# Kernel tuning notes

Measured on AMD Instinct MI355X. Metric: run time of the kernel, lower is better.

## Reference

```python
import jax, jax.numpy as jnp
import numpy as np

N = 10000      # nodes
E = 160000     # edges (before self-loops)
H = 8          # heads
D_IN, D_H1, D_H2 = 165, 128, 1    # per-head channels of gat1 / gat2
HID = H * D_H1                    # 1024


def batchnorm(x, gamma, beta, eps=1e-5):
    # training-mode BatchNorm1d: biased batch statistics over the node axis
    mu = x.mean(0)
    var = x.var(0)
    return (x - mu) * jax.lax.rsqrt(var + eps) * gamma + beta


def gatv2(x, src, dst, Wl, bl, Wr, br, att, bias, heads, out_ch, concat, n_nodes):
    # PyG GATv2Conv: lin_l on source, lin_r on target; e = att . LeakyReLU(xl_j + xr_i)
    xl = (x @ Wl + bl).reshape(n_nodes, heads, out_ch)   # source transform
    xr = (x @ Wr + br).reshape(n_nodes, heads, out_ch)   # target transform
    e = jax.nn.leaky_relu(xl[src] + xr[dst], 0.2)        # [E,H,C]
    logits = jnp.einsum('ehc,hc->eh', e, att)            # [E,H]
    # segment softmax over incoming edges of each destination node
    m = jax.lax.stop_gradient(jax.ops.segment_max(logits, dst, num_segments=n_nodes))
    a = jnp.exp(logits - m[dst])
    s = jax.ops.segment_sum(a, dst, num_segments=n_nodes)
    alpha = a / (s[dst] + 1e-16)                          # [E,H]
    out = jax.ops.segment_sum(xl[src] * alpha[..., None], dst, num_segments=n_nodes)
    out = out.reshape(n_nodes, heads * out_ch) if concat else out.mean(1)
    return out + bias


def setup_inputs() -> dict:
    key = jax.random.key(0)
    ks = jax.random.split(key, 12)
    g = lambda k, shape, fan_in: jax.random.normal(k, shape, jnp.float32) * (1.0 / np.sqrt(fan_in))
    return {
        'x': jax.random.normal(ks[0], (N, D_IN), jnp.float32),
        'gamma1': jnp.ones((D_IN,), jnp.float32),
        'beta1': jnp.zeros((D_IN,), jnp.float32),
        'Wl1': g(ks[1], (D_IN, HID), D_IN),
        'bl1': jnp.zeros((HID,), jnp.float32),
        'Wr1': g(ks[2], (D_IN, HID), D_IN),
        'br1': jnp.zeros((HID,), jnp.float32),
        'att1': g(ks[3], (H, D_H1), D_H1),
        'bias1': jnp.zeros((HID,), jnp.float32),
        'gamma2': jnp.ones((HID,), jnp.float32),
        'beta2': jnp.zeros((HID,), jnp.float32),
        'Wl2': g(ks[4], (HID, H * D_H2), HID),
        'bl2': jnp.zeros((H * D_H2,), jnp.float32),
        'Wr2': g(ks[5], (HID, H * D_H2), HID),
        'br2': jnp.zeros((H * D_H2,), jnp.float32),
        'att2': g(ks[6], (H, D_H2), D_H2),
        'bias2': jnp.zeros((D_H2,), jnp.float32),
        'edge_index': jax.random.randint(ks[7], (2, E), 0, N, jnp.int64 if jax.config.jax_enable_x64 else jnp.int32),
    }


def reference(x, gamma1, beta1, Wl1, bl1, Wr1, br1, att1, bias1,
              gamma2, beta2, Wl2, bl2, Wr2, br2, att2, bias2, edge_index):
    loops = jnp.arange(N, dtype=edge_index.dtype)
    src = jnp.concatenate([edge_index[0], loops])   # add_self_loops=True (PyG default)
    dst = jnp.concatenate([edge_index[1], loops])
    h = batchnorm(x, gamma1, beta1)
    h = gatv2(h, src, dst, Wl1, bl1, Wr1, br1, att1, bias1, H, D_H1, True, N)
    h = batchnorm(h, gamma2, beta2)
    h = jax.nn.leaky_relu(h, 0.01)                  # F.leaky_relu default slope
    out = gatv2(h, src, dst, Wl2, bl2, Wr2, br2, att2, bias2, H, D_H2, False, N)
    return out
```

## Files before the change

### kernel.cpp

```cpp
#include <hip/hip_runtime.h>

#define NN   10000
#define E0   160000
#define ET   170000
#define DIN  165
#define KP   192
#define HID  1024
#define NH   8
#define BP   200
#define K2P  1032
#define YT   2


typedef __bf16 bf16x8 __attribute__((ext_vector_type(8)));
typedef float  f32x4  __attribute__((ext_vector_type(4)));
typedef float  f32x2  __attribute__((ext_vector_type(2)));

__device__ __forceinline__ float bf2f(unsigned short u) {
    unsigned int i = ((unsigned int)u) << 16;
    return __builtin_bit_cast(float, i);
}
__device__ __forceinline__ unsigned short f2bf(float f) {
    unsigned int i = __builtin_bit_cast(unsigned int, f);
    i += 0x7fffu + ((i >> 16) & 1u);
    return (unsigned short)(i >> 16);
}
__device__ __forceinline__ float fin(float x) {
    return fminf(fmaxf(x, -1e30f), 1e30f);
}
__device__ __forceinline__ int clampi(int s) {
    return min(max(s, 0), NN - 1);
}
__device__ __forceinline__ void unpack8(uint4 u, float* f) {
    f[0]=bf2f((unsigned short)(u.x)); f[1]=bf2f((unsigned short)(u.x>>16));
    f[2]=bf2f((unsigned short)(u.y)); f[3]=bf2f((unsigned short)(u.y>>16));
    f[4]=bf2f((unsigned short)(u.z)); f[5]=bf2f((unsigned short)(u.z>>16));
    f[6]=bf2f((unsigned short)(u.w)); f[7]=bf2f((unsigned short)(u.w>>16));
}
__device__ __forceinline__ f32x2 up2(unsigned int u) {
    f32x2 r;
    r.x = __builtin_bit_cast(float, u << 16);
    r.y = __builtin_bit_cast(float, u & 0xffff0000u);
    return r;
}

__global__ __launch_bounds__(256) void debug_fill(float* __restrict__ out, float val) {
    int i = blockIdx.x * 256 + threadIdx.x;
    if (i < NN) out[i] = val;
}

__global__ __launch_bounds__(256) void fuseA_kernel(const float* __restrict__ x,
                                                    float* __restrict__ colsum, float* __restrict__ colsq,
                                                    const int* __restrict__ ei, int* __restrict__ deg) {
    const int b = blockIdx.x;
    if (b < 125) {
        int c = threadIdx.x;
        if (c >= DIN) return;
        int r0 = b * 80;
        float a0=0,a1=0,a2=0,a3=0, q0=0,q1=0,q2=0,q3=0;
        for (int r = r0; r < r0 + 80; r += 4) {
            float v0 = x[(size_t)r * DIN + c];
            float v1 = x[(size_t)(r + 1) * DIN + c];
            float v2 = x[(size_t)(r + 2) * DIN + c];
            float v3 = x[(size_t)(r + 3) * DIN + c];
            a0 += v0; q0 += v0 * v0;
            a1 += v1; q1 += v1 * v1;
            a2 += v2; q2 += v2 * v2;
            a3 += v3; q3 += v3 * v3;
        }
        atomicAdd(&colsum[c], (a0 + a1) + (a2 + a3));
        atomicAdd(&colsq[c],  (q0 + q1) + (q2 + q3));
    } else {
        int e = (b - 125) * 256 + threadIdx.x;
        if (e >= ET) return;
        int d = (e < E0) ? ei[E0 + e] : (e - E0);
        atomicAdd(&deg[clampi(d)], 1);
    }
}

__global__ __launch_bounds__(1024) void fuseB_kernel(
    const int* __restrict__ deg,
    int* __restrict__ offs, int* __restrict__ cur, int* __restrict__ perm,
    const float* __restrict__ x,
    const float* __restrict__ colsum, const float* __restrict__ colsq,
    const float* __restrict__ gamma, const float* __restrict__ beta,
    unsigned short* __restrict__ hn) {
    if (blockIdx.x != 0) {
        int idx = (blockIdx.x - 1) * 1024 + threadIdx.x;
        if (idx >= NN * KP) return;
        int r = idx / KP, c = idx - r * KP;
        float v = 0.f;
        if (c < DIN) {
            float mu  = colsum[c] * (1.f / NN);
            float var = fmaxf(colsq[c] * (1.f / NN) - mu * mu, 0.f);
            float a = gamma[c] * rsqrtf(var + 1e-5f);
            float b = beta[c] - mu * a;
            v = fin(x[(size_t)r * DIN + c] * a + b);
        }
        hn[idx] = f2bf(v);
        return;
    }
    __shared__ int wsum[16];
    __shared__ int bins[64];
    __shared__ int bcur[64];
    const int tid = threadIdx.x;
    const int base = tid * 10;
    int loc[10];
    int run = 0;
    #pragma unroll
    for (int j = 0; j < 10; ++j) {
        int idx = base + j;
        int v = (idx < NN) ? deg[idx] : 0;
        loc[j] = run;
        run += v;
    }
    const int lane = tid & 63;
    const int w = tid >> 6;
    int inc = run;
    #pragma unroll
    for (int s = 1; s < 64; s <<= 1) {
        int t = __shfl_up(inc, s);
        if (lane >= s) inc += t;
    }
    if (lane == 63) wsum[w] = inc;
    if (tid < 64) bins[tid] = 0;
    __syncthreads();
    int woff = 0;
    #pragma unroll
    for (int k = 0; k < 16; ++k) woff += (k < w) ? wsum[k] : 0;
    const int toff = woff + inc - run;
    #pragma unroll
    for (int j = 0; j < 10; ++j) {
        int idx = base + j;
        if (idx < NN) {
            int e = toff + loc[j]; offs[idx] = e; cur[idx] = e;
            atomicAdd(&bins[63 - min(deg[idx], 63)], 1);
        }
    }
    if (tid == 1023) offs[NN] = woff + inc;
    __syncthreads();
    if (tid < 64) {
        int v = bins[tid];
        int binc = v;
        #pragma unroll
        for (int s = 1; s < 64; s <<= 1) {
            int t = __shfl_up(binc, s);
            if (tid >= s) binc += t;
        }
        bcur[tid] = binc - v;
    }
    __syncthreads();
    #pragma unroll
    for (int j = 0; j < 10; ++j) {
        int idx = base + j;
        if (idx < NN) {
            int pos = atomicAdd(&bcur[63 - min(deg[idx], 63)], 1);
            perm[pos] = idx;
        }
    }
}

__global__ __launch_bounds__(256) void fuseC_kernel(const float* __restrict__ wl,
                                                    const float* __restrict__ wr,
                                                    unsigned short* __restrict__ wlt,
                                                    unsigned short* __restrict__ wrt,
                                                    const int* __restrict__ ei,
                                                    int* __restrict__ cur, int* __restrict__ ssrc) {
    const int b = blockIdx.x;
    if (b < 192) {
        const int z  = b / 96;
        const int rm = b - z * 96;
        const int ky = rm / 6;
        const int kx = rm - ky * 6;
        const float* src    = z ? wr  : wl;
        unsigned short* dst = z ? wrt : wlt;
        __shared__ float ts[32][65];
        const int k0 = kx * 32;
        const int n0 = ky * 64;
        const int tid = threadIdx.x;
        for (int idx = tid; idx < 32 * 64; idx += 256) {
            int k = idx >> 6, n = idx & 63;
            ts[k][n] = (k0 + k < DIN) ? src[(size_t)(k0 + k) * HID + n0 + n] : 0.f;
        }
        __syncthreads();
        for (int idx = tid; idx < 64 * 32; idx += 256) {
            int n = idx >> 5, k = idx & 31;
            dst[(size_t)(n0 + n) * KP + k0 + k] = f2bf(ts[k][n]);
        }
    } else {
        int e = (b - 192) * 256 + threadIdx.x;
        if (e >= ET) return;
        int s, d;
        if (e < E0) { s = ei[e]; d = ei[E0 + e]; }
        else        { s = e - E0; d = e - E0; }
        int pos = atomicAdd(&cur[clampi(d)], 1);
        if (pos >= 0 && pos < ET) ssrc[pos] = clampi(s);
    }
}

__global__ __launch_bounds__(256) void gemm1_kernel(
    const unsigned short* __restrict__ hn,
    const unsigned short* __restrict__ wlt,
    const unsigned short* __restrict__ wrt,
    const float* __restrict__ bl,
    const float* __restrict__ br,
    unsigned short* __restrict__ xl,
    unsigned short* __restrict__ xr) {
    __shared__ unsigned short bs[2][64 * BP];
    const int tid  = threadIdx.x;
    const int lane = tid & 63;
    const int wave = tid >> 6;
    const int col  = lane & 15;
    const int q    = lane >> 4;

    const int mbase = blockIdx.x * 128 + wave * 32;
    const int am0 = mbase + col;
    const int am1 = am0 + 16;
    const bool aok0 = (am0 < NN), aok1 = (am1 < NN);

    bf16x8 A0[6], A1[6];
    #pragma unroll
    for (int kt = 0; kt < 6; ++kt) {
        const int kk = kt * 32 + q * 8;
        uint4 a0u = make_uint4(0u,0u,0u,0u), a1u = make_uint4(0u,0u,0u,0u);
        if (aok0) a0u = *(const uint4*)(hn + (size_t)am0 * KP + kk);
        if (aok1) a1u = *(const uint4*)(hn + (size_t)am1 * KP + kk);
        A0[kt] = __builtin_bit_cast(bf16x8, a0u);
        A1[kt] = __builtin_bit_cast(bf16x8, a1u);
    }

    const int mblk = blockIdx.x * 128;

    #pragma unroll
    for (int yt = 0; yt < YT; ++yt) {
        const int n0 = (blockIdx.y * YT + yt) * 64;
        if (yt) __syncthreads();

        for (int idx = tid; idx < 64 * 48 * 2; idx += 256) {
            int z = idx >= 64 * 48;
            int rem = z ? idx - 64 * 48 : idx;
            int r = rem / 48, c = rem - r * 48;
            const unsigned short* wt = z ? wrt : wlt;
            uint2 v = *(const uint2*)(wt + (size_t)(n0 + r) * KP + c * 4);
            *(uint2*)&bs[z][r * BP + c * 4] = v;
        }
        __syncthreads();

        f32x4 accL[2][4], accR[2][4];
        #pragma unroll
        for (int m = 0; m < 2; ++m)
            for (int nt = 0; nt < 4; ++nt)
                for (int r = 0; r < 4; ++r) { accL[m][nt][r] = 0.f; accR[m][nt][r] = 0.f; }

        #pragma unroll
        for (int kt = 0; kt < 6; ++kt) {
            const int kk = kt * 32 + q * 8;
            #pragma unroll
            for (int nt = 0; nt < 4; ++nt) {
                bf16x8 bfl = __builtin_bit_cast(bf16x8, *(const uint4*)&bs[0][(nt * 16 + col) * BP + kk]);
                accL[0][nt] = __builtin_amdgcn_mfma_f32_16x16x32_bf16(A0[kt], bfl, accL[0][nt], 0, 0, 0);
                accL[1][nt] = __builtin_amdgcn_mfma_f32_16x16x32_bf16(A1[kt], bfl, accL[1][nt], 0, 0, 0);
                bf16x8 bfr = __builtin_bit_cast(bf16x8, *(const uint4*)&bs[1][(nt * 16 + col) * BP + kk]);
                accR[0][nt] = __builtin_amdgcn_mfma_f32_16x16x32_bf16(A0[kt], bfr, accR[0][nt], 0, 0, 0);
                accR[1][nt] = __builtin_amdgcn_mfma_f32_16x16x32_bf16(A1[kt], bfr, accR[1][nt], 0, 0, 0);
            }
        }

        __syncthreads();
        unsigned short* cl = &bs[0][0];
        unsigned short* cr = cl + 128 * 72;
        #pragma unroll
        for (int nt = 0; nt < 4; ++nt) {
            const int nc = n0 + nt * 16 + col;
            const float bLv = bl[nc];
            const float bRv = br[nc];
            #pragma unroll
            for (int m = 0; m < 2; ++m) {
                #pragma unroll
                for (int r = 0; r < 4; ++r) {
                    const int lrow = wave * 32 + m * 16 + q * 4 + r;
                    cl[lrow * 72 + nt * 16 + col] = f2bf(fin(accL[m][nt][r] + bLv));
                    cr[lrow * 72 + nt * 16 + col] = f2bf(fin(accR[m][nt][r] + bRv));
                }
            }
        }
        __syncthreads();
        for (int t = tid; t < 128 * 8; t += 256) {
            const int row = t >> 3, ch = t & 7;
            const int grow = mblk + row;
            if (grow < NN) {
                *(uint4*)(xl + (size_t)grow * HID + n0 + ch * 8) = *(const uint4*)&cl[row * 72 + ch * 8];
                *(uint4*)(xr + (size_t)grow * HID + n0 + ch * 8) = *(const uint4*)&cr[row * 72 + ch * 8];
            }
        }
    }
}

__global__ __launch_bounds__(256) void gat1_node(
    const unsigned short* __restrict__ xl1, const unsigned short* xr1,
    const float* __restrict__ att1, const float* __restrict__ bias1,
    const int* __restrict__ offs, const int* __restrict__ ssrc,
    const int* __restrict__ perm,
    unsigned short* agg) {
    const int lane = threadIdx.x & 63;
    const int wave = threadIdx.x >> 6;
    const int i = perm[blockIdx.x * 4 + wave];
    const int e0 = offs[i];
    const int e1 = max(offs[i + 1], e0);

    f32x2 xr2[8], at2[8], o2[8];
    {
        const uint4* xp = (const uint4*)(xr1 + (size_t)i * HID + lane * 16);
        uint4 u0 = xp[0], u1 = xp[1];
        unsigned int w[8] = {u0.x, u0.y, u0.z, u0.w, u1.x, u1.y, u1.z, u1.w};
        const float4* ap = (const float4*)(att1 + lane * 16);
        float4 a0 = ap[0], a1 = ap[1], a2 = ap[2], a3 = ap[3];
        float af[16] = {a0.x,a0.y,a0.z,a0.w, a1.x,a1.y,a1.z,a1.w,
                        a2.x,a2.y,a2.z,a2.w, a3.x,a3.y,a3.z,a3.w};
        #pragma unroll
        for (int j = 0; j < 8; ++j) {
            xr2[j] = up2(w[j]);
            at2[j].x = af[2*j]; at2[j].y = af[2*j+1];
            o2[j].x = 0.f; o2[j].y = 0.f;
        }
    }
    float s = 0.f;

    int e = e0;
    for (; e + 1 < e1; e += 2) {
        const int s0i = clampi(ssrc[e]);
        const int s1i = clampi(ssrc[e + 1]);
        const uint4* xp0 = (const uint4*)(xl1 + (size_t)s0i * HID + lane * 16);
        const uint4* xp1 = (const uint4*)(xl1 + (size_t)s1i * HID + lane * 16);
        uint4 a0 = xp0[0], a1 = xp0[1], b0 = xp1[0], b1 = xp1[1];
        unsigned int wa[8] = {a0.x,a0.y,a0.z,a0.w, a1.x,a1.y,a1.z,a1.w};
        unsigned int wb[8] = {b0.x,b0.y,b0.z,b0.w, b1.x,b1.y,b1.z,b1.w};
        f32x2 xa[8], xb[8];
        #pragma unroll
        for (int j = 0; j < 8; ++j) { xa[j] = up2(wa[j]); xb[j] = up2(wb[j]); }
        f32x2 pa = {0.f, 0.f}, pb = {0.f, 0.f};
        #pragma unroll
        for (int j = 0; j < 8; ++j) {
            f32x2 va = xa[j] + xr2[j];
            f32x2 vb = xb[j] + xr2[j];
            va = __builtin_elementwise_max(va, 0.2f * va);
            vb = __builtin_elementwise_max(vb, 0.2f * vb);
            pa = __builtin_elementwise_fma(at2[j], va, pa);
            pb = __builtin_elementwise_fma(at2[j], vb, pb);
        }
        float p0 = pa.x + pa.y;
        float p1 = pb.x + pb.y;
        p0 += __shfl_xor(p0, 1); p0 += __shfl_xor(p0, 2); p0 += __shfl_xor(p0, 4);
        p1 += __shfl_xor(p1, 1); p1 += __shfl_xor(p1, 2); p1 += __shfl_xor(p1, 4);
        const float aa0 = __expf(fminf(fin(p0), 50.f));
        const float aa1 = __expf(fminf(fin(p1), 50.f));
        s += aa0 + aa1;
        f32x2 av0; av0.x = aa0; av0.y = aa0;
        f32x2 av1; av1.x = aa1; av1.y = aa1;
        #pragma unroll
        for (int j = 0; j < 8; ++j)
            o2[j] = __builtin_elementwise_fma(av0, xa[j],
                    __builtin_elementwise_fma(av1, xb[j], o2[j]));
    }
    if (e < e1) {
        const int sidx = clampi(ssrc[e]);
        const uint4* xp = (const uint4*)(xl1 + (size_t)sidx * HID + lane * 16);
        uint4 u0 = xp[0], u1 = xp[1];
        unsigned int w[8] = {u0.x,u0.y,u0.z,u0.w, u1.x,u1.y,u1.z,u1.w};
        f32x2 xv[8];
        #pragma unroll
        for (int j = 0; j < 8; ++j) xv[j] = up2(w[j]);
        f32x2 p2 = {0.f, 0.f};
        #pragma unroll
        for (int j = 0; j < 8; ++j) {
            f32x2 v = xv[j] + xr2[j];
            v = __builtin_elementwise_max(v, 0.2f * v);
            p2 = __builtin_elementwise_fma(at2[j], v, p2);
        }
        float p = p2.x + p2.y;
        p += __shfl_xor(p, 1); p += __shfl_xor(p, 2); p += __shfl_xor(p, 4);
        const float a = __expf(fminf(fin(p), 50.f));
        s += a;
        f32x2 av; av.x = a; av.y = a;
        #pragma unroll
        for (int j = 0; j < 8; ++j)
            o2[j] = __builtin_elementwise_fma(av, xv[j], o2[j]);
    }

    const float inv = 1.f / (s + 1e-16f);
    const float4* bp = (const float4*)(bias1 + lane * 16);
    float4 b0 = bp[0], b1 = bp[1], b2 = bp[2], b3 = bp[3];
    float bb[16] = {b0.x,b0.y,b0.z,b0.w, b1.x,b1.y,b1.z,b1.w,
                    b2.x,b2.y,b2.z,b2.w, b3.x,b3.y,b3.z,b3.w};
    unsigned short ov[16];
    #pragma unroll
    for (int j = 0; j < 8; ++j) {
        ov[2*j]   = f2bf(fin(o2[j].x * inv + bb[2*j]));
        ov[2*j+1] = f2bf(fin(o2[j].y * inv + bb[2*j+1]));
    }
    uint4* op = (uint4*)(agg + (size_t)i * HID + lane * 16);
    op[0] = *(const uint4*)&ov[0];
    op[1] = *(const uint4*)&ov[8];
}

__global__ __launch_bounds__(256) void bn2_stats(const unsigned short* __restrict__ agg,
                                                 float* __restrict__ colsum, float* __restrict__ colsq) {
    int r0 = blockIdx.x * 80;
    int t = threadIdx.x;
    float s0=0,s1=0,s2=0,s3=0,q0=0,q1=0,q2=0,q3=0;
    #pragma unroll 2
    for (int r = r0; r < r0 + 80; ++r) {
        const ushort4 u = *(const ushort4*)(agg + (size_t)r * HID + t * 4);
        float v0=bf2f(u.x), v1=bf2f(u.y), v2=bf2f(u.z), v3=bf2f(u.w);
        s0+=v0; q0+=v0*v0; s1+=v1; q1+=v1*v1;
        s2+=v2; q2+=v2*v2; s3+=v3; q3+=v3*v3;
    }
    atomicAdd(&colsum[t*4+0], s0); atomicAdd(&colsq[t*4+0], q0);
    atomicAdd(&colsum[t*4+1], s1); atomicAdd(&colsq[t*4+1], q1);
    atomicAdd(&colsum[t*4+2], s2); atomicAdd(&colsq[t*4+2], q2);
    atomicAdd(&colsum[t*4+3], s3); atomicAdd(&colsq[t*4+3], q3);
}

__global__ __launch_bounds__(256) void gemm2_kernel(
    const unsigned short* __restrict__ agg,
    const float* __restrict__ colsum, const float* __restrict__ colsq,
    const float* __restrict__ gamma, const float* __restrict__ beta,
    const float* __restrict__ wl2, const float* __restrict__ wr2,
    const float* __restrict__ bl2, const float* __restrict__ br2,
    float* __restrict__ xl2, float* __restrict__ xr2) {
    __shared__ unsigned short bs[16 * K2P];
    __shared__ float a2s[HID], b2s[HID];
    __shared__ float red[4 * 64 * 4];
    const int tid  = threadIdx.x;
    const int lane = tid & 63;
    const int wave = tid >> 6;
    const int col  = lane & 15;
    const int q    = lane >> 4;

    for (int idx = tid; idx < 16 * HID; idx += 256) {
        int n = idx >> 10, k = idx & (HID - 1);
        float v = (n < 8) ? wl2[k * 8 + n] : wr2[k * 8 + (n - 8)];
        bs[n * K2P + k] = f2bf(v);
    }
    for (int cc = tid; cc < HID; cc += 256) {
        float mu  = colsum[cc] * (1.f / NN);
        float var = fmaxf(colsq[cc] * (1.f / NN) - mu * mu, 0.f);
        float a = gamma[cc] * rsqrtf(var + 1e-5f);
        a2s[cc] = a; b2s[cc] = beta[cc] - mu * a;
    }
    __syncthreads();

    const int m0 = blockIdx.x * 16;
    const int am = m0 + col;

    f32x4 acc;
    acc[0] = acc[1] = acc[2] = acc[3] = 0.f;
    #pragma unroll
    for (int t = 0; t < 8; ++t) {
        const int kt = wave * 8 + t;
        const int kk = kt * 32 + q * 8;
        uint4 u = *(const uint4*)(agg + (size_t)am * HID + kk);
        float xv[8];
        unpack8(u, xv);
        unsigned short hv[8];
        #pragma unroll
        for (int j = 0; j < 8; ++j) {
            float v = xv[j] * a2s[kk + j] + b2s[kk + j];
            v = fmaxf(v, 0.01f * v);
            hv[j] = f2bf(fin(v));
        }
        bf16x8 af = __builtin_bit_cast(bf16x8, *(const uint4*)hv);
        bf16x8 bf = __builtin_bit_cast(bf16x8, *(const uint4*)&bs[col * K2P + kk]);
        acc = __builtin_amdgcn_mfma_f32_16x16x32_bf16(af, bf, acc, 0, 0, 0);
    }

    *(f32x4*)&red[(wave * 64 + lane) * 4] = acc;
    __syncthreads();
    if (wave == 0) {
        f32x4 a0 = *(const f32x4*)&red[lane * 4];
        f32x4 a1 = *(const f32x4*)&red[(64 + lane) * 4];
        f32x4 a2 = *(const f32x4*)&red[(128 + lane) * 4];
        f32x4 a3 = *(const f32x4*)&red[(192 + lane) * 4];
        acc = (a0 + a1) + (a2 + a3);
        const float bv = (col < 8) ? bl2[col] : br2[col - 8];
        float* outp = (col < 8) ? (xl2 + col) : (xr2 + (col - 8));
        #pragma unroll
        for (int r = 0; r < 4; ++r) {
            const int row = m0 + q * 4 + r;
            outp[row * 8] = fin(acc[r] + bv);
        }
    }
}

__global__ __launch_bounds__(256) void gat2_node(
    const float* __restrict__ xl2, const float* __restrict__ xr2,
    const float* __restrict__ att2, const float* __restrict__ bias2,
    const int* __restrict__ offs, const int* __restrict__ ssrc,
    const int* __restrict__ perm,
    float* __restrict__ out) {
    const int lane = threadIdx.x & 63;
    const int wave = threadIdx.x >> 6;
    const int i = perm[blockIdx.x * 4 + wave];
    const int h = lane & 7, slot = lane >> 3;
    const int e0 = offs[i];
    const int e1 = max(offs[i + 1], e0);
    const float xr_h = xr2[i * 8 + h];
    const float att_h = att2[h];
    float ssum = 0.f, wsum = 0.f;
    for (int eb = e0; eb < e1; eb += 8) {
        int e = eb + slot;
        if (e < e1) {
            float xlv = xl2[clampi(ssrc[e]) * 8 + h];
            float v = xlv + xr_h;
            v = fmaxf(v, 0.2f * v);
            float a = __expf(fminf(fin(att_h * v), 50.f));
            ssum += a; wsum += a * xlv;
        }
    }
    ssum += __shfl_xor(ssum, 8); ssum += __shfl_xor(ssum, 16); ssum += __shfl_xor(ssum, 32);
    wsum += __shfl_xor(wsum, 8); wsum += __shfl_xor(wsum, 16); wsum += __shfl_xor(wsum, 32);
    float v = fin(wsum / (ssum + 1e-16f));
    v += __shfl_xor(v, 1); v += __shfl_xor(v, 2); v += __shfl_xor(v, 4);
    if (lane == 0) out[i] = fin(v * 0.125f + bias2[0]);
}

extern "C" void kernel_launch(void* const* d_in, const int* in_sizes, int n_in,
                              void* d_out, int out_size, void* d_ws, size_t ws_size,
                              hipStream_t stream) {
    float* out = (float*)d_out;

    static const int expected[18] = {
        NN * DIN, DIN, DIN, DIN * HID, HID, DIN * HID, HID, HID, HID,
        HID, HID, HID * NH, NH, HID * NH, NH, NH, 1, 2 * E0
    };
    if (n_in != 18) {
        debug_fill<<<(NN + 255) / 256, 256, 0, stream>>>(out, 8192.f + 64.f * (float)n_in);
        return;
    }
    for (int i = 0; i < 18; ++i) {
        if (in_sizes[i] != expected[i]) {
            debug_fill<<<(NN + 255) / 256, 256, 0, stream>>>(out, 4096.f + 32.f * (float)i);
            return;
        }
    }

    const float* x      = (const float*)d_in[0];
    const float* gamma1 = (const float*)d_in[1];
    const float* beta1  = (const float*)d_in[2];
    const float* Wl1    = (const float*)d_in[3];
    const float* bl1    = (const float*)d_in[4];
    const float* Wr1    = (const float*)d_in[5];
    const float* br1    = (const float*)d_in[6];
    const float* att1   = (const float*)d_in[7];
    const float* bias1  = (const float*)d_in[8];
    const float* gamma2 = (const float*)d_in[9];
    const float* beta2  = (const float*)d_in[10];
    const float* Wl2    = (const float*)d_in[11];
    const float* bl2    = (const float*)d_in[12];
    const float* Wr2    = (const float*)d_in[13];
    const float* br2    = (const float*)d_in[14];
    const float* att2   = (const float*)d_in[15];
    const float* bias2  = (const float*)d_in[16];
    const int*   ei     = (const int*)d_in[17];

    char* p = (char*)d_ws;
    auto alloc = [&](size_t bytes) -> void* {
        void* r = (void*)p;
        p += (bytes + 255) & ~(size_t)255;
        return r;
    };
    unsigned short* xl1  = (unsigned short*)alloc((size_t)NN * HID * 2);
    unsigned short* xr1  = (unsigned short*)alloc((size_t)NN * HID * 2);
    unsigned short* agg  = xr1;
    unsigned short* hn   = (unsigned short*)alloc((size_t)NN * KP * 2);
    unsigned short* wlt  = (unsigned short*)alloc((size_t)HID * KP * 2);
    unsigned short* wrt  = (unsigned short*)alloc((size_t)HID * KP * 2);
    float*          xl2  = (float*)alloc((size_t)NN * 8 * 4);
    float*          xr2  = (float*)alloc((size_t)NN * 8 * 4);
    int*            offs = (int*)alloc((NN + 1) * 4);
    int*            cur  = (int*)alloc(NN * 4);
    int*            ssrc = (int*)alloc(ET * 4);
    int*            perm = (int*)alloc(NN * 4);
    char* zbase = p;
    float* colsum1 = (float*)alloc(DIN * 4);
    float* colsq1  = (float*)alloc(DIN * 4);
    float* colsum2 = (float*)alloc(HID * 4);
    float* colsq2  = (float*)alloc(HID * 4);
    int*   deg     = (int*)alloc(NN * 4);
    size_t zlen = (size_t)(p - zbase);
    hipMemsetAsync(zbase, 0, zlen, stream);

    fuseA_kernel<<<125 + (ET + 255) / 256, 256, 0, stream>>>(x, colsum1, colsq1, ei, deg);
    fuseB_kernel<<<1 + (NN * KP + 1023) / 1024, 1024, 0, stream>>>(
        deg, offs, cur, perm, x, colsum1, colsq1, gamma1, beta1, hn);
    fuseC_kernel<<<192 + (ET + 255) / 256, 256, 0, stream>>>(Wl1, Wr1, wlt, wrt, ei, cur, ssrc);
    gemm1_kernel<<<dim3((NN + 127) / 128, HID / 64 / YT), 256, 0, stream>>>(
        hn, wlt, wrt, bl1, br1, xl1, xr1);
    gat1_node<<<NN / 4, 256, 0, stream>>>(xl1, xr1, att1, bias1, offs, ssrc, perm, agg);
    bn2_stats<<<125, 256, 0, stream>>>(agg, colsum2, colsq2);
    gemm2_kernel<<<NN / 16, 256, 0, stream>>>(agg, colsum2, colsq2, gamma2, beta2,
                                              Wl2, Wr2, bl2, br2, xl2, xr2);
    gat2_node<<<NN / 4, 256, 0, stream>>>(xl2, xr2, att2, bias2, offs, ssrc, perm, out);
}
```

Before: 294.8 us.

## Restructure gemm1 tiling: weights in registers, activation tile staged in LDS

Rewrites the first GEMM so each block computes a 64-row by 128-column tile of either the left or right projection. Each wave now keeps its B (weight) fragments in registers and reads A rows from a shared-memory tile, where before A lived in registers and both weight matrices were staged through LDS. The grid becomes 157x16 blocks, which is meant to raise parallelism and cut LDS traffic per MFMA. The cost is that each weight slice is reloaded by many more blocks, and the output staging uses a new padded LDS layout.

```diff
diff --git a/kernel.cpp b/kernel.cpp
--- a/kernel.cpp
+++ b/kernel.cpp
@@ -7,9 +7,9 @@
 #define KP   192
 #define HID  1024
 #define NH   8
-#define BP   200
+#define AP   200
+#define CP   136
 #define K2P  1032
-#define YT   2
 
 
 typedef __bf16 bf16x8 __attribute__((ext_vector_type(8)));
@@ -206,92 +206,100 @@
     const float* __restrict__ br,
     unsigned short* __restrict__ xl,
     unsigned short* __restrict__ xr) {
-    __shared__ unsigned short bs[2][64 * BP];
+    __shared__ unsigned short as[64 * AP];
     const int tid  = threadIdx.x;
     const int lane = tid & 63;
     const int wave = tid >> 6;
     const int col  = lane & 15;
     const int q    = lane >> 4;
 
-    const int mbase = blockIdx.x * 128 + wave * 32;
-    const int am0 = mbase + col;
-    const int am1 = am0 + 16;
-    const bool aok0 = (am0 < NN), aok1 = (am1 < NN);
-
-    bf16x8 A0[6], A1[6];
+    const int m0 = blockIdx.x * 64;
+    const int z  = blockIdx.y >> 3;
+    const int nb = (blockIdx.y & 7) * 128;
+    const unsigned short* wt = z ? wrt : wlt;
+
+    bf16x8 B[2][6];
+    {
+        const int bc0 = nb + wave * 32 + col;
+        #pragma unroll
+        for (int nt = 0; nt < 2; ++nt) {
+            const unsigned short* wp = wt + (size_t)(bc0 + nt * 16) * KP + q * 8;
+            #pragma unroll
+            for (int kt = 0; kt < 6; ++kt)
+                B[nt][kt] = __builtin_bit_cast(bf16x8, *(const uint4*)(wp + kt * 32));
+        }
+    }
+
+    {
+        const int r  = tid >> 2;
+        const int s0 = (tid & 3) * 48;
+        const int grow = m0 + r;
+        uint4 t0 = {0,0,0,0}, t1 = t0, t2 = t0, t3 = t0, t4 = t0, t5 = t0;
+        if (grow < NN) {
+            const unsigned short* gp = hn + (size_t)grow * KP + s0;
+            t0 = *(const uint4*)(gp);
+            t1 = *(const uint4*)(gp + 8);
+            t2 = *(const uint4*)(gp + 16);
+            t3 = *(const uint4*)(gp + 24);
+            t4 = *(const uint4*)(gp + 32);
+            t5 = *(const uint4*)(gp + 40);
+        }
+        unsigned short* lp = as + r * AP + s0;
+        *(uint4*)(lp)      = t0;
+        *(uint4*)(lp + 8)  = t1;
+        *(uint4*)(lp + 16) = t2;
+        *(uint4*)(lp + 24) = t3;
+        *(uint4*)(lp + 32) = t4;
+        *(uint4*)(lp + 40) = t5;
+    }
+    __syncthreads();
+
+    f32x4 acc[4][2];
+    #pragma unroll
+    for (int mi = 0; mi < 4; ++mi)
+        for (int nt = 0; nt < 2; ++nt)
+            acc[mi][nt][0] = acc[mi][nt][1] = acc[mi][nt][2] = acc[mi][nt][3] = 0.f;
+
     #pragma unroll
     for (int kt = 0; kt < 6; ++kt) {
         const int kk = kt * 32 + q * 8;
-        uint4 a0u = make_uint4(0u,0u,0u,0u), a1u = make_uint4(0u,0u,0u,0u);
-        if (aok0) a0u = *(const uint4*)(hn + (size_t)am0 * KP + kk);
-        if (aok1) a1u = *(const uint4*)(hn + (size_t)am1 * KP + kk);
-        A0[kt] = __builtin_bit_cast(bf16x8, a0u);
-        A1[kt] = __builtin_bit_cast(bf16x8, a1u);
-    }
-
-    const int mblk = blockIdx.x * 128;
-
-    #pragma unroll
-    for (int yt = 0; yt < YT; ++yt) {
-        const int n0 = (blockIdx.y * YT + yt) * 64;
-        if (yt) __syncthreads();
-
-        for (int idx = tid; idx < 64 * 48 * 2; idx += 256) {
-            int z = idx >= 64 * 48;
-            int rem = z ? idx - 64 * 48 : idx;
-            int r = rem / 48, c = rem - r * 48;
-            const unsigned short* wt = z ? wrt : wlt;
-            uint2 v = *(const uint2*)(wt + (size_t)(n0 + r) * KP + c * 4);
-            *(uint2*)&bs[z][r * BP + c * 4] = v;
-        }
-        __syncthreads();
-
-        f32x4 accL[2][4], accR[2][4];
-        #pragma unroll
-        for (int m = 0; m < 2; ++m)
-            for (int nt = 0; nt < 4; ++nt)
-                for (int r = 0; r < 4; ++r) { accL[m][nt][r] = 0.f; accR[m][nt][r] = 0.f; }
-
-        #pragma unroll
-        for (int kt = 0; kt < 6; ++kt) {
-            const int kk = kt * 32 + q * 8;
+        bf16x8 A[4];
+        #pragma unroll
+        for (int mi = 0; mi < 4; ++mi)
+            A[mi] = __builtin_bit_cast(bf16x8, *(const uint4*)(as + (mi * 16 + col) * AP + kk));
+        #pragma unroll
+        for (int mi = 0; mi < 4; ++mi) {
+            acc[mi][0] = __builtin_amdgcn_mfma_f32_16x16x32_bf16(A[mi], B[0][kt], acc[mi][0], 0, 0, 0);
+            acc[mi][1] = __builtin_amdgcn_mfma_f32_16x16x32_bf16(A[mi], B[1][kt], acc[mi][1], 0, 0, 0);
+        }
+    }
+
+    __syncthreads();
+    #pragma unroll
+    for (int nt = 0; nt < 2; ++nt) {
+        const int lc = wave * 32 + nt * 16 + col;
+        const float bv = (z ? br : bl)[nb + lc];
+        #pragma unroll
+        for (int mi = 0; mi < 4; ++mi) {
             #pragma unroll
-            for (int nt = 0; nt < 4; ++nt) {
-                bf16x8 bfl = __builtin_bit_cast(bf16x8, *(const uint4*)&bs[0][(nt * 16 + col) * BP + kk]);
-                accL[0][nt] = __builtin_amdgcn_mfma_f32_16x16x32_bf16(A0[kt], bfl, accL[0][nt], 0, 0, 0);
-                accL[1][nt] = __builtin_amdgcn_mfma_f32_16x16x32_bf16(A1[kt], bfl, accL[1][nt], 0, 0, 0);
-                bf16x8 bfr = __builtin_bit_cast(bf16x8, *(const uint4*)&bs[1][(nt * 16 + col) * BP + kk]);
-                accR[0][nt] = __builtin_amdgcn_mfma_f32_16x16x32_bf16(A0[kt], bfr, accR[0][nt], 0, 0, 0);
-                accR[1][nt] = __builtin_amdgcn_mfma_f32_16x16x32_bf16(A1[kt], bfr, accR[1][nt], 0, 0, 0);
+            for (int r = 0; r < 4; ++r) {
+                const int lr = mi * 16 + q * 4 + r;
+                as[lr * CP + lc] = f2bf(fin(acc[mi][nt][r] + bv));
             }
         }
-
-        __syncthreads();
-        unsigned short* cl = &bs[0][0];
-        unsigned short* cr = cl + 128 * 72;
-        #pragma unroll
-        for (int nt = 0; nt < 4; ++nt) {
-            const int nc = n0 + nt * 16 + col;
-            const float bLv = bl[nc];
-            const float bRv = br[nc];
-            #pragma unroll
-            for (int m = 0; m < 2; ++m) {
-                #pragma unroll
-                for (int r = 0; r < 4; ++r) {
-                    const int lrow = wave * 32 + m * 16 + q * 4 + r;
-                    cl[lrow * 72 + nt * 16 + col] = f2bf(fin(accL[m][nt][r] + bLv));
-                    cr[lrow * 72 + nt * 16 + col] = f2bf(fin(accR[m][nt][r] + bRv));
-                }
-            }
-        }
-        __syncthreads();
-        for (int t = tid; t < 128 * 8; t += 256) {
-            const int row = t >> 3, ch = t & 7;
-            const int grow = mblk + row;
-            if (grow < NN) {
-                *(uint4*)(xl + (size_t)grow * HID + n0 + ch * 8) = *(const uint4*)&cl[row * 72 + ch * 8];
-                *(uint4*)(xr + (size_t)grow * HID + n0 + ch * 8) = *(const uint4*)&cr[row * 72 + ch * 8];
-            }
+    }
+    __syncthreads();
+    {
+        const int r  = tid >> 2;
+        const int sg = (tid & 3) * 32;
+        const int grow = m0 + r;
+        if (grow < NN) {
+            unsigned short* dst = (z ? xr : xl) + (size_t)grow * HID + nb + sg;
+            const unsigned short* sp = as + r * CP + sg;
+            *(uint4*)(dst)      = *(const uint4*)(sp);
+            *(uint4*)(dst + 8)  = *(const uint4*)(sp + 8);
+            *(uint4*)(dst + 16) = *(const uint4*)(sp + 16);
+            *(uint4*)(dst + 24) = *(const uint4*)(sp + 24);
         }
     }
 }
@@ -594,8 +602,7 @@
     fuseB_kernel<<<1 + (NN * KP + 1023) / 1024, 1024, 0, stream>>>(
         deg, offs, cur, perm, x, colsum1, colsq1, gamma1, beta1, hn);
     fuseC_kernel<<<192 + (ET + 255) / 256, 256, 0, stream>>>(Wl1, Wr1, wlt, wrt, ei, cur, ssrc);
-    gemm1_kernel<<<dim3((NN + 127) / 128, HID / 64 / YT), 256, 0, stream>>>(
-        hn, wlt, wrt, bl1, br1, xl1, xr1);
+    gemm1_kernel<<<dim3((NN + 63) / 64, 16), 256, 0, stream>>>(hn, wlt, wrt, bl1, br1, xl1, xr1);
     gat1_node<<<NN / 4, 256, 0, stream>>>(xl1, xr1, att1, bias1, offs, ssrc, perm, agg);
     bn2_stats<<<125, 256, 0, stream>>>(agg, colsum2, colsq2);
     gemm2_kernel<<<NN / 16, 256, 0, stream>>>(agg, colsum2, colsq2, gamma2, beta2,
```

New measurement: 275.3 us. -6.6%, faster.
